# Optimization experiments

Measured on AMD Instinct MI355X. Metric: run time of the kernel, lower is better.

The kernel has to match this reference:

```python
import jax, jax.numpy as jnp
import numpy as np

LOSS_WEIGHT = 1.0


def _norm_gram(feat):
    # feat: [B, C, H, W] -> normalized channel gram [B, C, C]
    B, C, H, W = feat.shape
    F = feat.reshape(B, C, H * W)                      # [B, C, HW]
    gram = jnp.einsum('bcn,bdn->bcd', F, F)            # [B, C, C]
    n = jnp.sqrt(jnp.sum(F * F, axis=2))               # [B, C] per-channel L2 norm
    norm_M = n[:, :, None] * n[:, None, :]             # [B, C, C]
    return gram / norm_M


def setup_inputs() -> dict:
    key = jax.random.key(0)
    k1, k2 = jax.random.split(key)
    det = jax.random.normal(k1, (8, 512, 128, 128), dtype=jnp.float32)
    sr = jax.random.normal(k2, (8, 512, 128, 128), dtype=jnp.float32)
    return {"det": det, "sr": sr}


def reference(det, sr):
    sm_det = _norm_gram(det)
    sm_sr = _norm_gram(sr)
    # use_l2=True -> MSELoss (mean reduction); weighted_loss with weight=None,
    # reduction='mean' on a scalar is identity; then * loss_weight.
    loss = jnp.mean((sm_det - sm_sr) ** 2)
    return loss * LOSS_WEIGHT
```

## Files before the change

kernel.cpp:

```cpp
#include <hip/hip_runtime.h>
#include <hip/hip_bf16.h>

#define C_CH 512
#define HW 16384
#define NB 8
#define TILE 128
#define BK 32
#define NTB 4
#define NTILES 10
#define KSPLIT 8
#define KCHUNK (HW / KSPLIT)
#define KSTEPS (KCHUNK / BK)
#define NGRAM 16
#define CC (C_CH * C_CH)
#define LOSS_BLOCKS 1024
#define GRID (NGRAM * KSPLIT * NTILES)
#define PANEL_V8 (TILE * BK / 8)

typedef float f32x4 __attribute__((ext_vector_type(4)));
typedef float f32x8 __attribute__((ext_vector_type(8)));
typedef __bf16 bf16x8 __attribute__((ext_vector_type(8)));

__device__ __forceinline__ int slot_of(int R, int c) {
    return (R >> 1) * 8 + ((((R & 1) << 2) + c) ^ ((R >> 1) & 7));
}

__global__ __launch_bounds__(256, 3) void gram_kernel(const float* __restrict__ det,
                                                      const float* __restrict__ sr,
                                                      float* __restrict__ gram) {
    const int lbid = ((int)blockIdx.x & 7) * (GRID / 8) + ((int)blockIdx.x >> 3);
    const int t = lbid % NTILES;
    const int gk = lbid / NTILES;
    const int ks = gk & (KSPLIT - 1);
    const int g = gk >> 3;
    const int tensor = g >> 3, b = g & 7;

    int ti = 0, tt = t;
    while (tt >= NTB - ti) { tt -= NTB - ti; ++ti; }
    const int tj = ti + tt;
    const bool diag = (ti == tj);

    const float* F = (tensor ? sr : det) + (size_t)b * C_CH * HW;
    const float* Abase = F + (size_t)(ti * TILE) * HW + ks * KCHUNK;
    const float* Bbase = F + (size_t)(tj * TILE) * HW + ks * KCHUNK;

    __shared__ bf16x8 lds[4 * PANEL_V8];

    const int tid = threadIdx.x;
    const int lane = tid & 63;
    const int wid = tid >> 6;
    const int wr = wid >> 1, wc = wid & 1;

    int goff[2], lslot[2];
    #pragma unroll
    for (int q = 0; q < 2; ++q) {
        int c = q * 256 + tid;
        int r = c >> 2, ch = c & 3;
        goff[q] = r * HW + ch * 8;
        lslot[q] = slot_of(r, ch);
    }

    f32x8 va[2], vb[2];
    auto LOAD = [&](int kt) {
        const int ko = kt * BK;
        #pragma unroll
        for (int q = 0; q < 2; ++q) va[q] = *(const f32x8*)(Abase + goff[q] + ko);
        if (!diag) {
            #pragma unroll
            for (int q = 0; q < 2; ++q) vb[q] = *(const f32x8*)(Bbase + goff[q] + ko);
        }
    };
    auto WRITE = [&](int buf) {
        bf16x8* As = lds + buf * 2 * PANEL_V8;
        #pragma unroll
        for (int q = 0; q < 2; ++q) {
            bf16x8 h;
            #pragma unroll
            for (int i = 0; i < 8; ++i) h[i] = (__bf16)va[q][i];
            As[lslot[q]] = h;
        }
        if (!diag) {
            bf16x8* Bs = As + PANEL_V8;
            #pragma unroll
            for (int q = 0; q < 2; ++q) {
                bf16x8 h;
                #pragma unroll
                for (int i = 0; i < 8; ++i) h[i] = (__bf16)vb[q][i];
                Bs[lslot[q]] = h;
            }
        }
    };

    f32x4 acc[4][4] = {};
    const int kg = lane >> 4;
    const int l15 = lane & 15;
    auto COMPUTE = [&](int buf) {
        const bf16x8* As = lds + buf * 2 * PANEL_V8;
        const bf16x8* Bs = diag ? As : As + PANEL_V8;
        bf16x8 af[4], bfr[4];
        #pragma unroll
        for (int m = 0; m < 4; ++m) {
            int R = wr * 64 + m * 16 + l15;
            af[m] = As[slot_of(R, kg)];
        }
        #pragma unroll
        for (int n = 0; n < 4; ++n) {
            int R = wc * 64 + n * 16 + l15;
            bfr[n] = Bs[slot_of(R, kg)];
        }
        #pragma unroll
        for (int m = 0; m < 4; ++m)
            #pragma unroll
            for (int n = 0; n < 4; ++n)
                if (!diag || (wc * 64 + n * 16 + 16 > wr * 64 + m * 16))
                    acc[m][n] = __builtin_amdgcn_mfma_f32_16x16x32_bf16(af[m], bfr[n], acc[m][n], 0, 0, 0);
    };

    LOAD(0);
    WRITE(0);
    __syncthreads();
    int cur = 0;
    #pragma unroll 1
    for (int kt = 0; kt < KSTEPS; ++kt) {
        if (kt + 1 < KSTEPS) LOAD(kt + 1);
        COMPUTE(cur);
        if (kt + 1 < KSTEPS) WRITE(cur ^ 1);
        __syncthreads();
        cur ^= 1;
    }

    float* gout = gram + (size_t)g * CC;
    const int rb = ti * TILE + wr * 64 + (kg << 2);
    const int cb = tj * TILE + wc * 64 + l15;
    #pragma unroll
    for (int m = 0; m < 4; ++m)
        #pragma unroll
        for (int n = 0; n < 4; ++n) {
            if (diag && (wc * 64 + n * 16 + 16 <= wr * 64 + m * 16)) continue;
            #pragma unroll
            for (int j = 0; j < 4; ++j)
                atomicAdd(&gout[(size_t)(rb + m * 16 + j) * C_CH + cb + n * 16], acc[m][n][j]);
        }
}

__global__ void norm_kernel(const float* __restrict__ gram, float* __restrict__ invn) {
    const int g = blockIdx.x, c = threadIdx.x;
    float v = gram[(size_t)g * CC + (size_t)c * C_CH + c];
    invn[g * C_CH + c] = 1.0f / sqrtf(v);
}

__global__ __launch_bounds__(256) void loss_kernel(const float* __restrict__ gram,
                                                   const float* __restrict__ invn,
                                                   float* __restrict__ partials) {
    const int tid = threadIdx.x;
    float s = 0.f;
    for (int idx = blockIdx.x * 256 + tid; idx < NB * CC; idx += LOSS_BLOCKS * 256) {
        int b = idx >> 18;
        int c = (idx >> 9) & 511;
        int d = idx & 511;
        int cc = c, dd = d;
        if (dd < cc) { int tmp = cc; cc = dd; dd = tmp; }
        float gd = gram[(size_t)b * CC + (size_t)cc * C_CH + dd];
        float gs = gram[(size_t)(8 + b) * CC + (size_t)cc * C_CH + dd];
        float sd = gd * invn[b * C_CH + c] * invn[b * C_CH + d];
        float ss = gs * invn[(8 + b) * C_CH + c] * invn[(8 + b) * C_CH + d];
        float diff = sd - ss;
        s += diff * diff;
    }
    #pragma unroll
    for (int off = 32; off > 0; off >>= 1) s += __shfl_down(s, off, 64);
    __shared__ float red[4];
    if ((tid & 63) == 0) red[tid >> 6] = s;
    __syncthreads();
    if (tid == 0) partials[blockIdx.x] = red[0] + red[1] + red[2] + red[3];
}

__global__ void final_kernel(const float* __restrict__ partials, float* __restrict__ out) {
    const int tid = threadIdx.x;
    float s = 0.f;
    for (int i = tid; i < LOSS_BLOCKS; i += 256) s += partials[i];
    #pragma unroll
    for (int off = 32; off > 0; off >>= 1) s += __shfl_down(s, off, 64);
    __shared__ float red[4];
    if ((tid & 63) == 0) red[tid >> 6] = s;
    __syncthreads();
    if (tid == 0) out[0] = (red[0] + red[1] + red[2] + red[3]) * (1.0f / (float)(NB * (size_t)CC));
}

extern "C" void kernel_launch(void* const* d_in, const int* in_sizes, int n_in,
                              void* d_out, int out_size, void* d_ws, size_t ws_size,
                              hipStream_t stream) {
    const float* det = (const float*)d_in[0];
    const float* sr  = (const float*)d_in[1];
    float* gram     = (float*)d_ws;
    float* invn     = gram + (size_t)NGRAM * CC;
    float* partials = invn + NGRAM * C_CH;
    float* out      = (float*)d_out;

    hipMemsetAsync(gram, 0, (size_t)NGRAM * CC * sizeof(float), stream);
    gram_kernel<<<GRID, 256, 0, stream>>>(det, sr, gram);
    norm_kernel<<<NGRAM, C_CH, 0, stream>>>(gram, invn);
    loss_kernel<<<LOSS_BLOCKS, 256, 0, stream>>>(gram, invn, partials);
    final_kernel<<<1, 256, 0, stream>>>(partials, out);
}
```

Before: 257.5 us.

## Pre-convert inputs to bf16, then run gram GEMM with direct global-to-LDS loads

Adds a separate pass that converts both fp32 inputs into one bf16 workspace buffer. A new gram kernel then streams bf16 panels straight into LDS through global_load_lds, with BK raised to 64, XOR-swizzled slots, vmcnt-based double buffering and raised MFMA priority. The goal is to halve the bytes the GEMM re-reads and to drop the per-thread register convert and LDS write path. In exchange it costs an extra full read/write pass over the inputs. It only runs when the workspace can hold the bf16 copy; otherwise it falls back to the old fp32 kernel.

```diff
diff --git a/kernel.cpp b/kernel.cpp
--- a/kernel.cpp
+++ b/kernel.cpp
@@ -5,29 +5,170 @@
 #define HW 16384
 #define NB 8
 #define TILE 128
-#define BK 32
 #define NTB 4
 #define NTILES 10
 #define KSPLIT 8
 #define KCHUNK (HW / KSPLIT)
-#define KSTEPS (KCHUNK / BK)
 #define NGRAM 16
 #define CC (C_CH * C_CH)
 #define LOSS_BLOCKS 1024
 #define GRID (NGRAM * KSPLIT * NTILES)
-#define PANEL_V8 (TILE * BK / 8)
+
+#define BKB 64
+#define KSTEPS_B (KCHUNK / BKB)
+#define BKF 32
+#define KSTEPS_F (KCHUNC_F)
+#define KCHUNC_F (KCHUNK / BKF)
+#define PANEL_V8 (TILE * BKF / 8)
+
+#define TOT_ELEMS 134217728LL
+#define HALF_ELEMS 67108864LL
 
 typedef float f32x4 __attribute__((ext_vector_type(4)));
 typedef float f32x8 __attribute__((ext_vector_type(8)));
 typedef __bf16 bf16x8 __attribute__((ext_vector_type(8)));
 
+#define GLOAD_LDS16(gsrc, ldst)                                                 \
+    __builtin_amdgcn_global_load_lds(                                           \
+        (const __attribute__((address_space(1))) void*)(gsrc),                  \
+        (__attribute__((address_space(3))) void*)(ldst), 16, 0, 0)
+
+#define BAR_LGKM()                                                  \
+    do {                                                            \
+        asm volatile("s_waitcnt lgkmcnt(0)" ::: "memory");          \
+        __builtin_amdgcn_s_barrier();                               \
+        asm volatile("" ::: "memory");                              \
+    } while (0)
+
+__global__ __launch_bounds__(256) void convert_kernel(const float* __restrict__ det,
+                                                      const float* __restrict__ sr,
+                                                      __bf16* __restrict__ bf) {
+    const long long stride = (long long)gridDim.x * 256 * 8;
+    for (long long i = ((long long)blockIdx.x * 256 + threadIdx.x) * 8;
+         i < TOT_ELEMS; i += stride) {
+        const float* src = (i < HALF_ELEMS) ? det + i : sr + (i - HALF_ELEMS);
+        f32x4 lo = *(const f32x4*)src;
+        f32x4 hi = *(const f32x4*)(src + 4);
+        bf16x8 h;
+        #pragma unroll
+        for (int k = 0; k < 4; ++k) { h[k] = (__bf16)lo[k]; h[4 + k] = (__bf16)hi[k]; }
+        *(bf16x8*)(bf + i) = h;
+    }
+}
+
+__global__ __launch_bounds__(256, 2) void gram_bf16_kernel(const __bf16* __restrict__ bf,
+                                                           float* __restrict__ gram) {
+    const int bid = (int)blockIdx.x;
+    const int lbid = (bid & 7) * (GRID / 8) + (bid >> 3);
+    const int t = lbid % NTILES;
+    const int gk = lbid / NTILES;
+    const int ks = gk & (KSPLIT - 1);
+    const int g = gk >> 3;
+
+    int ti = 0, tt = t;
+    while (tt >= NTB - ti) { tt -= NTB - ti; ++ti; }
+    const int tj = ti + tt;
+    const bool diag = (ti == tj);
+
+    const __bf16* F = bf + (size_t)g * C_CH * HW;
+    const __bf16* Abase = F + (size_t)(ti * TILE) * HW + ks * KCHUNK;
+    const __bf16* Bbase = F + (size_t)(tj * TILE) * HW + ks * KCHUNK;
+
+    __shared__ bf16x8 lds[2][2][1024];
+
+    const int tid = threadIdx.x;
+    const int lane = tid & 63;
+    const int wid = tid >> 6;
+    const int wr = wid >> 1, wc = wid & 1;
+    const int kg = lane >> 4;
+    const int l15 = lane & 15;
+
+    auto STAGE = [&](int buf, int kt) {
+        const __bf16* sA = Abase + kt * BKB;
+        #pragma unroll
+        for (int q = 0; q < 4; ++q) {
+            int f = q * 256 + tid;
+            int R = f >> 3, s = f & 7;
+            int c = s ^ (R & 7);
+            GLOAD_LDS16(sA + (size_t)R * HW + c * 8, &lds[buf][0][f]);
+        }
+        if (!diag) {
+            const __bf16* sB = Bbase + kt * BKB;
+            #pragma unroll
+            for (int q = 0; q < 4; ++q) {
+                int f = q * 256 + tid;
+                int R = f >> 3, s = f & 7;
+                int c = s ^ (R & 7);
+                GLOAD_LDS16(sB + (size_t)R * HW + c * 8, &lds[buf][1][f]);
+            }
+        }
+    };
+
+    f32x4 acc[4][4] = {};
+    auto COMPUTE = [&](int buf) {
+        const bf16x8* As = &lds[buf][0][0];
+        const bf16x8* Bs = diag ? As : &lds[buf][1][0];
+        #pragma unroll
+        for (int ksub = 0; ksub < 2; ++ksub) {
+            bf16x8 af[4], bfr[4];
+            #pragma unroll
+            for (int m = 0; m < 4; ++m) {
+                int R = wr * 64 + m * 16 + l15;
+                af[m] = As[R * 8 + ((ksub * 4 + kg) ^ (R & 7))];
+            }
+            #pragma unroll
+            for (int n = 0; n < 4; ++n) {
+                int R = wc * 64 + n * 16 + l15;
+                bfr[n] = Bs[R * 8 + ((ksub * 4 + kg) ^ (R & 7))];
+            }
+            __builtin_amdgcn_s_setprio(1);
+            #pragma unroll
+            for (int m = 0; m < 4; ++m)
+                #pragma unroll
+                for (int n = 0; n < 4; ++n)
+                    if (!diag || (wc * 64 + n * 16 + 16 > wr * 64 + m * 16))
+                        acc[m][n] = __builtin_amdgcn_mfma_f32_16x16x32_bf16(af[m], bfr[n], acc[m][n], 0, 0, 0);
+            __builtin_amdgcn_s_setprio(0);
+        }
+    };
+
+    STAGE(0, 0);
+    #pragma unroll 1
+    for (int kt = 0; kt < KSTEPS_B; ++kt) {
+        if (kt + 1 < KSTEPS_B) {
+            STAGE((kt + 1) & 1, kt + 1);
+            if (diag) asm volatile("s_waitcnt vmcnt(4)" ::: "memory");
+            else      asm volatile("s_waitcnt vmcnt(8)" ::: "memory");
+        } else {
+            asm volatile("s_waitcnt vmcnt(0)" ::: "memory");
+        }
+        __builtin_amdgcn_s_barrier();
+        asm volatile("" ::: "memory");
+        COMPUTE(kt & 1);
+        BAR_LGKM();
+    }
+
+    float* gout = gram + (size_t)g * CC;
+    const int rb = ti * TILE + wr * 64 + (kg << 2);
+    const int cb = tj * TILE + wc * 64 + l15;
+    #pragma unroll
+    for (int m = 0; m < 4; ++m)
+        #pragma unroll
+        for (int n = 0; n < 4; ++n) {
+            if (diag && (wc * 64 + n * 16 + 16 <= wr * 64 + m * 16)) continue;
+            #pragma unroll
+            for (int j = 0; j < 4; ++j)
+                atomicAdd(&gout[(size_t)(rb + m * 16 + j) * C_CH + cb + n * 16], acc[m][n][j]);
+        }
+}
+
 __device__ __forceinline__ int slot_of(int R, int c) {
     return (R >> 1) * 8 + ((((R & 1) << 2) + c) ^ ((R >> 1) & 7));
 }
 
-__global__ __launch_bounds__(256, 3) void gram_kernel(const float* __restrict__ det,
-                                                      const float* __restrict__ sr,
-                                                      float* __restrict__ gram) {
+__global__ __launch_bounds__(256, 2) void gram_f32_kernel(const float* __restrict__ det,
+                                                          const float* __restrict__ sr,
+                                                          float* __restrict__ gram) {
     const int lbid = ((int)blockIdx.x & 7) * (GRID / 8) + ((int)blockIdx.x >> 3);
     const int t = lbid % NTILES;
     const int gk = lbid / NTILES;
@@ -62,7 +203,7 @@
 
     f32x8 va[2], vb[2];
     auto LOAD = [&](int kt) {
-        const int ko = kt * BK;
+        const int ko = kt * BKF;
         #pragma unroll
         for (int q = 0; q < 2; ++q) va[q] = *(const f32x8*)(Abase + goff[q] + ko);
         if (!diag) {
@@ -94,20 +235,13 @@
     f32x4 acc[4][4] = {};
     const int kg = lane >> 4;
     const int l15 = lane & 15;
-    auto COMPUTE = [&](int buf) {
-        const bf16x8* As = lds + buf * 2 * PANEL_V8;
+    auto COMPUTE = [&](const bf16x8* As) {
         const bf16x8* Bs = diag ? As : As + PANEL_V8;
         bf16x8 af[4], bfr[4];
         #pragma unroll
-        for (int m = 0; m < 4; ++m) {
-            int R = wr * 64 + m * 16 + l15;
-            af[m] = As[slot_of(R, kg)];
-        }
-        #pragma unroll
-        for (int n = 0; n < 4; ++n) {
-            int R = wc * 64 + n * 16 + l15;
-            bfr[n] = Bs[slot_of(R, kg)];
-        }
+        for (int m = 0; m < 4; ++m) af[m] = As[slot_of(wr * 64 + m * 16 + l15, kg)];
+        #pragma unroll
+        for (int n = 0; n < 4; ++n) bfr[n] = Bs[slot_of(wc * 64 + n * 16 + l15, kg)];
         #pragma unroll
         for (int m = 0; m < 4; ++m)
             #pragma unroll
@@ -121,10 +255,10 @@
     __syncthreads();
     int cur = 0;
     #pragma unroll 1
-    for (int kt = 0; kt < KSTEPS; ++kt) {
-        if (kt + 1 < KSTEPS) LOAD(kt + 1);
-        COMPUTE(cur);
-        if (kt + 1 < KSTEPS) WRITE(cur ^ 1);
+    for (int kt = 0; kt < 64; ++kt) {
+        if (kt + 1 < 64) LOAD(kt + 1);
+        COMPUTE(lds + cur * 2 * PANEL_V8);
+        if (kt + 1 < 64) WRITE(cur ^ 1);
         __syncthreads();
         cur ^= 1;
     }
@@ -192,14 +326,33 @@
                               hipStream_t stream) {
     const float* det = (const float*)d_in[0];
     const float* sr  = (const float*)d_in[1];
-    float* gram     = (float*)d_ws;
-    float* invn     = gram + (size_t)NGRAM * CC;
-    float* partials = invn + NGRAM * C_CH;
-    float* out      = (float*)d_out;
-
-    hipMemsetAsync(gram, 0, (size_t)NGRAM * CC * sizeof(float), stream);
-    gram_kernel<<<GRID, 256, 0, stream>>>(det, sr, gram);
-    norm_kernel<<<NGRAM, C_CH, 0, stream>>>(gram, invn);
-    loss_kernel<<<LOSS_BLOCKS, 256, 0, stream>>>(gram, invn, partials);
-    final_kernel<<<1, 256, 0, stream>>>(partials, out);
-}
+    float* out = (float*)d_out;
+
+    const size_t bf_bytes   = (size_t)TOT_ELEMS * 2;
+    const size_t gram_bytes = (size_t)NGRAM * CC * sizeof(float);
+    const size_t aux_bytes  = (NGRAM * C_CH + LOSS_BLOCKS) * sizeof(float);
+
+    if (ws_size >= bf_bytes + gram_bytes + aux_bytes) {
+        __bf16* bfp     = (__bf16*)d_ws;
+        float* gram     = (float*)((char*)d_ws + bf_bytes);
+        float* invn     = gram + (size_t)NGRAM * CC;
+        float* partials = invn + NGRAM * C_CH;
+
+        convert_kernel<<<2048, 256, 0, stream>>>(det, sr, bfp);
+        hipMemsetAsync(gram, 0, gram_bytes, stream);
+        gram_bf16_kernel<<<GRID, 256, 0, stream>>>(bfp, gram);
+        norm_kernel<<<NGRAM, C_CH, 0, stream>>>(gram, invn);
+        loss_kernel<<<LOSS_BLOCKS, 256, 0, stream>>>(gram, invn, partials);
+        final_kernel<<<1, 256, 0, stream>>>(partials, out);
+    } else {
+        float* gram     = (float*)d_ws;
+        float* invn     = gram + (size_t)NGRAM * CC;
+        float* partials = invn + NGRAM * C_CH;
+
+        hipMemsetAsync(gram, 0, gram_bytes, stream);
+        gram_f32_kernel<<<GRID, 256, 0, stream>>>(det, sr, gram);
+        norm_kernel<<<NGRAM, C_CH, 0, stream>>>(gram, invn);
+        loss_kernel<<<LOSS_BLOCKS, 256, 0, stream>>>(gram, invn, partials);
+        final_kernel<<<1, 256, 0, stream>>>(partials, out);
+    }
+}
```

New measurement: 348.7 us. 1.35x slower.
